# Kernel tuning notes

Measured on AMD Instinct MI355X. Metric: run time of the kernel, lower is better.

Reference implementation:

```python
import jax, jax.numpy as jnp
import numpy as np

# Config matching init_kwargs: N=4 networks, dims 128 -> 1024 -> 1024 -> 512
A, B, D = 8, 2048, 128     # agents, batch, input size
N = 4                       # number of independent SePS networks
H1, H2, H3 = 1024, 1024, 512


def setup_inputs() -> dict:
    key = jax.random.key(0)
    ks = jax.random.split(key, 6)
    inputs = jax.random.normal(ks[0], (A, B, D), dtype=jnp.float32)  # stacked per-agent obs
    seps_indices = jax.random.randint(ks[1], (B, A), 0, N)           # cluster id per (sample, agent)
    scale = lambda k, shape, fan: jax.random.normal(k, shape, dtype=jnp.float32) * (1.0 / np.sqrt(fan))
    W0 = scale(ks[2], (N, D, H1), D);   b0 = jnp.zeros((N, H1), jnp.float32)
    W1 = scale(ks[3], (N, H1, H2), H1); b1 = jnp.zeros((N, H2), jnp.float32)
    W2 = scale(ks[4], (N, H2, H3), H2); b2 = jnp.zeros((N, H3), jnp.float32)
    return {"inputs": inputs, "seps_indices": seps_indices,
            "W0": W0, "b0": b0, "W1": W1, "b1": b1, "W2": W2, "b2": b2}


def reference(inputs, seps_indices, W0, b0, W1, b1, W2, b2):
    # Run every network densely on the full stacked input, as the torch module does.
    # inputs: [A, B, D]; W*: [N, in, out]
    h = jax.nn.relu(jnp.einsum('abd,ndh->nabh', inputs, W0) + b0[:, None, None, :])
    h = jax.nn.relu(jnp.einsum('nabh,nhk->nabk', h, W1) + b1[:, None, None, :])
    out_all = jnp.einsum('nabk,nko->nabo', h, W2) + b2[:, None, None, :]  # [N, A, B, H3]
    # Gather along the network axis per (agent, sample): seps_indices is [B, A]
    idx = seps_indices.T                              # [A, B]
    a = jnp.arange(inputs.shape[0])[:, None]          # [A, 1]
    b = jnp.arange(inputs.shape[1])[None, :]          # [1, B]
    return out_all[idx, a, b, :]                      # [A, B, H3] (stacked per-agent outputs)
```

## Files before the change

kernel.cpp:

```cpp
#include <hip/hip_runtime.h>
#include <hip/hip_bf16.h>

#define AG 8
#define BT 2048
#define RT (AG*BT)
#define NNET 4
#define D0 128
#define H1 1024
#define H2 1024
#define H3 512

typedef __attribute__((ext_vector_type(8))) short short8;
typedef __attribute__((ext_vector_type(4))) float f32x4;

#define VMWAIT(N) asm volatile("s_waitcnt vmcnt(" #N ")" ::: "memory")

__device__ __forceinline__ float bf2f(unsigned short u){
  return __uint_as_float(((unsigned int)u) << 16);
}
__device__ __forceinline__ unsigned short f2bf(float f){
  unsigned int x = __float_as_uint(f);
  x += 0x7fff + ((x >> 16) & 1);
  return (unsigned short)(x >> 16);
}

__device__ __forceinline__ void gload_lds16(const void* g, void* l){
  __builtin_amdgcn_global_load_lds(
      (const __attribute__((address_space(1))) unsigned int*)g,
      (__attribute__((address_space(3))) unsigned int*)l, 16, 0, 0);
}

__device__ __forceinline__ int bucket_off(const int* counts, int n){
  int s = 0;
  #pragma unroll
  for (int i = 0; i < NNET-1; i++) if (i < n) s += counts[i];
  return s;
}

__global__ void k_init(int* counts){
  if (threadIdx.x < NNET) counts[threadIdx.x] = 0;
}

__global__ __launch_bounds__(256) void k_compact(const int* __restrict__ seps,
                          int* __restrict__ counts, int* __restrict__ rowlist){
  __shared__ int lcount[NNET];
  __shared__ int lbase[NNET];
  int t = blockIdx.x * 256 + threadIdx.x;
  if (threadIdx.x < NNET) lcount[threadIdx.x] = 0;
  __syncthreads();
  int a = t >> 11, b = t & (BT-1);
  int n = seps[b*AG + a];
  int lrank = atomicAdd(&lcount[n], 1);
  __syncthreads();
  if (threadIdx.x < NNET)
    lbase[threadIdx.x] = atomicAdd(&counts[threadIdx.x], lcount[threadIdx.x]);
  __syncthreads();
  rowlist[n*RT + lbase[n] + lrank] = t;
}

template<int K, int NOUT>
__global__ __launch_bounds__(256) void k_transpose(const float* __restrict__ W,
                                                   unsigned short* __restrict__ WT){
  __shared__ float tile[32][33];
  int n = blockIdx.z;
  int k0 = blockIdx.x*32, o0 = blockIdx.y*32;
  const float* Wn = W + (size_t)n*K*NOUT;
  unsigned short* WTn = WT + (size_t)n*NOUT*K;
  int tx = threadIdx.x & 31, ty0 = threadIdx.x >> 5;
  #pragma unroll
  for (int r = 0; r < 32; r += 8)
    tile[ty0 + r][tx] = Wn[(size_t)(k0 + ty0 + r)*NOUT + o0 + tx];
  __syncthreads();
  #pragma unroll
  for (int r = 0; r < 32; r += 8)
    WTn[(size_t)(o0 + ty0 + r)*K + k0 + tx] = f2bf(tile[tx][ty0 + r]);
}

__global__ __launch_bounds__(256) void k_gather0(const float* __restrict__ X,
                          const int* __restrict__ counts,
                          const int* __restrict__ rowlist, unsigned short* __restrict__ X0h){
  int n = blockIdx.y;
  int cnt = counts[n];
  int i = blockIdx.x*16 + (threadIdx.x >> 4);
  if (i >= cnt) return;
  int off = bucket_off(counts, n);
  int orig = rowlist[n*RT + i];
  int c = (threadIdx.x & 15) * 8;
  const float* src = X + (size_t)orig*D0 + c;
  float4 v0 = *(const float4*)src, v1 = *(const float4*)(src+4);
  ushort4 u0, u1;
  u0.x=f2bf(v0.x); u0.y=f2bf(v0.y); u0.z=f2bf(v0.z); u0.w=f2bf(v0.w);
  u1.x=f2bf(v1.x); u1.y=f2bf(v1.y); u1.z=f2bf(v1.z); u1.w=f2bf(v1.w);
  unsigned short* dst = X0h + (size_t)(off + i)*D0 + c;
  *(ushort4*)dst = u0; *(ushort4*)(dst+4) = u1;
}

template<int K, int NOUT, int RELU, int SCATTER>
__global__ __launch_bounds__(256) void k_mlp(
    const unsigned short* __restrict__ X,
    const unsigned short* __restrict__ WT,
    const float* __restrict__ Bias,
    const int* __restrict__ counts,
    const int* __restrict__ rowlist,
    unsigned short* __restrict__ Yh,
    float* __restrict__ Yf)
{
  constexpr int T = K / 32;
  const int n = blockIdx.z;
  const int cnt = counts[n];
  const int i0 = blockIdx.x * 128;
  if (i0 >= cnt) return;
  const int off = bucket_off(counts, n);
  const int bn = blockIdx.y * 128;

  __shared__ __align__(16) unsigned short As[3][128*32];
  __shared__ __align__(16) unsigned short Bs[3][128*32];
  __shared__ int rs[128];

  const int t = threadIdx.x, lane = t & 63, wave = t >> 6;
  const int wm = wave >> 1, wn = wave & 1;
  const int lr = lane & 15, g = lane >> 4;

  if (SCATTER && t < 128) rs[t] = rowlist[n*RT + min(i0 + t, cnt-1)];

  const unsigned short* pA[2]; const unsigned short* pB[2];
  unsigned int ldsoff[2];
  const unsigned short* WTn = WT + (size_t)n * NOUT * K;
  #pragma unroll
  for (int j = 0; j < 2; j++){
    int r  = (j*4 + wave)*16 + (lane >> 2);
    int ps = lane & 3;
    int ls = ps ^ ((r >> 1) & 3);
    int rA = min(i0 + r, cnt-1);
    pA[j] = X   + (size_t)(off + rA)*K + ls*8;
    pB[j] = WTn + (size_t)(bn  + r )*K + ls*8;
    ldsoff[j] = (unsigned)(j*4 + wave) * 512;
  }

  int aoff[4], boff[4];
  #pragma unroll
  for (int i = 0; i < 4; i++){
    int ra = wm*64 + i*16 + lr;
    aoff[i] = ra*32 + (g ^ ((ra>>1)&3))*8;
    int rb = wn*64 + i*16 + lr;
    boff[i] = rb*32 + (g ^ ((rb>>1)&3))*8;
  }

  __syncthreads();

  #pragma unroll
  for (int s = 0; s < 3; ++s){
    #pragma unroll
    for (int j = 0; j < 2; j++){
      gload_lds16(pA[j], &As[s][ldsoff[j]]);
      gload_lds16(pB[j], &Bs[s][ldsoff[j]]);
      pA[j] += 32; pB[j] += 32;
    }
  }

  f32x4 acc[4][4] = {};
  int b = 0;
  for (int ks = 0; ks < T; ++ks){
    if (ks < T-2)       VMWAIT(8);
    else if (ks == T-2) VMWAIT(4);
    else                VMWAIT(0);
    __builtin_amdgcn_s_barrier();

    short8 av[4], bv[4];
    #pragma unroll
    for (int i = 0; i < 4; i++) av[i] = *(const short8*)&As[b][aoff[i]];
    #pragma unroll
    for (int i = 0; i < 4; i++) bv[i] = *(const short8*)&Bs[b][boff[i]];
    asm volatile("s_waitcnt lgkmcnt(0)" ::: "memory");
    __builtin_amdgcn_sched_barrier(0);
    __builtin_amdgcn_s_barrier();

    if (ks + 3 < T){
      #pragma unroll
      for (int j = 0; j < 2; j++){
        gload_lds16(pA[j], &As[b][ldsoff[j]]);
        gload_lds16(pB[j], &Bs[b][ldsoff[j]]);
        pA[j] += 32; pB[j] += 32;
      }
    }

    __builtin_amdgcn_s_setprio(1);
    #pragma unroll
    for (int mi = 0; mi < 4; mi++)
      #pragma unroll
      for (int ni = 0; ni < 4; ni++)
        acc[mi][ni] = __builtin_amdgcn_mfma_f32_16x16x32_bf16(bv[ni], av[mi], acc[mi][ni], 0, 0, 0);
    __builtin_amdgcn_s_setprio(0);

    b = (b == 2) ? 0 : b + 1;
  }

  f32x4 bias4[4];
  #pragma unroll
  for (int ni = 0; ni < 4; ni++)
    bias4[ni] = *(const f32x4*)&Bias[n*NOUT + bn + wn*64 + ni*16 + g*4];

  #pragma unroll
  for (int mi = 0; mi < 4; mi++){
    int rloc = wm*64 + mi*16 + lr;
    int grow = i0 + rloc;
    if (grow < cnt){
      #pragma unroll
      for (int ni = 0; ni < 4; ni++){
        float o[4];
        #pragma unroll
        for (int i = 0; i < 4; i++){
          float v = acc[mi][ni][i] + bias4[ni][i];
          if (RELU) v = fmaxf(v, 0.f);
          o[i] = v;
        }
        int cb = bn + wn*64 + ni*16 + (g<<2);
        if (SCATTER){
          *(float4*)&Yf[(size_t)rs[rloc]*NOUT + cb] = make_float4(o[0],o[1],o[2],o[3]);
        } else {
          ushort4 u;
          u.x=f2bf(o[0]); u.y=f2bf(o[1]); u.z=f2bf(o[2]); u.w=f2bf(o[3]);
          *(ushort4*)&Yh[(size_t)(off + grow)*NOUT + cb] = u;
        }
      }
    }
  }
}

extern "C" void kernel_launch(void* const* d_in, const int* in_sizes, int n_in,
                              void* d_out, int out_size, void* d_ws, size_t ws_size,
                              hipStream_t stream) {
  const float* inputs = (const float*)d_in[0];
  const int*   seps   = (const int*)  d_in[1];
  const float* W0     = (const float*)d_in[2];
  const float* b0     = (const float*)d_in[3];
  const float* W1     = (const float*)d_in[4];
  const float* b1     = (const float*)d_in[5];
  const float* W2     = (const float*)d_in[6];
  const float* b2     = (const float*)d_in[7];
  float* out = (float*)d_out;

  char* ws = (char*)d_ws;
  int* counts  = (int*)ws;
  int* rowlist = (int*)(ws + 4096);
  const size_t MB = 1u << 20;
  unsigned short* WT0 = (unsigned short*)(ws + 1*MB);
  unsigned short* WT1 = (unsigned short*)(ws + 2*MB);
  unsigned short* WT2 = (unsigned short*)(ws + 10*MB);
  unsigned short* h1  = (unsigned short*)(ws + 14*MB);
  unsigned short* h2  = (unsigned short*)(ws + 46*MB);
  unsigned short* X0h = (unsigned short*)(ws + 46*MB);

  k_init   <<<1, 64, 0, stream>>>(counts);
  k_compact<<<RT/256, 256, 0, stream>>>(seps, counts, rowlist);

  k_transpose<D0, H1><<<dim3(D0/32, H1/32, NNET), 256, 0, stream>>>(W0, WT0);
  k_transpose<H1, H2><<<dim3(H1/32, H2/32, NNET), 256, 0, stream>>>(W1, WT1);
  k_transpose<H2, H3><<<dim3(H2/32, H3/32, NNET), 256, 0, stream>>>(W2, WT2);
  k_gather0<<<dim3(RT/16, NNET), 256, 0, stream>>>(inputs, counts, rowlist, X0h);

  k_mlp<D0, H1, 1, 0><<<dim3(RT/128, H1/128, NNET), 256, 0, stream>>>(
      X0h, WT0, b0, counts, rowlist, h1, nullptr);
  k_mlp<H1, H2, 1, 0><<<dim3(RT/128, H2/128, NNET), 256, 0, stream>>>(
      h1, WT1, b1, counts, rowlist, h2, nullptr);
  k_mlp<H2, H3, 0, 1><<<dim3(RT/128, H3/128, NNET), 256, 0, stream>>>(
      h2, WT2, b2, counts, rowlist, nullptr, out);
}
```

Measured before the change: 152.1 us.

## Enlarge GEMM tiles to 256-row blocks with 8 waves and templated warp layout

Generalizes the grouped MLP GEMM kernel to 512-thread blocks covering 256 rows and a configurable 256- or 128-column tile, with a templated wave grid and per-thread load counts. Layers 1 and 2 use 256x256 tiles with a 2x4 wave grid, and layer 3 uses 256x128 tiles with 4x2. The aim is more operand reuse from LDS and fewer global loads per MFMA. In exchange it uses more LDS and accumulator registers per block, which can lower occupancy. It also pads more rows in the partial last tile of each network bucket.

```diff
diff --git a/kernel.cpp b/kernel.cpp
--- a/kernel.cpp
+++ b/kernel.cpp
@@ -13,8 +13,6 @@
 typedef __attribute__((ext_vector_type(8))) short short8;
 typedef __attribute__((ext_vector_type(4))) float f32x4;
 
-#define VMWAIT(N) asm volatile("s_waitcnt vmcnt(" #N ")" ::: "memory")
-
 __device__ __forceinline__ float bf2f(unsigned short u){
   return __uint_as_float(((unsigned int)u) << 16);
 }
@@ -22,6 +20,14 @@
   unsigned int x = __float_as_uint(f);
   x += 0x7fff + ((x >> 16) & 1);
   return (unsigned short)(x >> 16);
+}
+
+template<int N> __device__ __forceinline__ void vmw(){
+  if constexpr (N==8)      asm volatile("s_waitcnt vmcnt(8)" ::: "memory");
+  else if constexpr (N==6) asm volatile("s_waitcnt vmcnt(6)" ::: "memory");
+  else if constexpr (N==4) asm volatile("s_waitcnt vmcnt(4)" ::: "memory");
+  else if constexpr (N==3) asm volatile("s_waitcnt vmcnt(3)" ::: "memory");
+  else                     asm volatile("s_waitcnt vmcnt(0)" ::: "memory");
 }
 
 __device__ __forceinline__ void gload_lds16(const void* g, void* l){
@@ -95,8 +101,8 @@
   *(ushort4*)dst = u0; *(ushort4*)(dst+4) = u1;
 }
 
-template<int K, int NOUT, int RELU, int SCATTER>
-__global__ __launch_bounds__(256) void k_mlp(
+template<int K, int NOUT, int BN, int WMW, int WNW, int RELU, int SCATTER>
+__global__ __launch_bounds__(512) void k_mlp(
     const unsigned short* __restrict__ X,
     const unsigned short* __restrict__ WT,
     const float* __restrict__ Bias,
@@ -105,44 +111,57 @@
     unsigned short* __restrict__ Yh,
     float* __restrict__ Yf)
 {
-  constexpr int T = K / 32;
+  constexpr int T  = K / 32;
+  constexpr int MF = 256 / WMW / 16;
+  constexpr int NF = BN  / WNW / 16;
+  constexpr int LA = 2;
+  constexpr int LB = (BN*32*2) / (512*16);
+  constexpr int LPT = LA + LB;
+
   const int n = blockIdx.z;
   const int cnt = counts[n];
-  const int i0 = blockIdx.x * 128;
+  const int i0 = blockIdx.x * 256;
   if (i0 >= cnt) return;
   const int off = bucket_off(counts, n);
-  const int bn = blockIdx.y * 128;
-
-  __shared__ __align__(16) unsigned short As[3][128*32];
-  __shared__ __align__(16) unsigned short Bs[3][128*32];
-  __shared__ int rs[128];
+  const int bn = blockIdx.y * BN;
+
+  __shared__ __align__(16) unsigned short As[3][256*32];
+  __shared__ __align__(16) unsigned short Bs[3][BN*32];
+  __shared__ int rs[256];
 
   const int t = threadIdx.x, lane = t & 63, wave = t >> 6;
-  const int wm = wave >> 1, wn = wave & 1;
+  const int wm = wave / WNW, wn = wave % WNW;
   const int lr = lane & 15, g = lane >> 4;
 
-  if (SCATTER && t < 128) rs[t] = rowlist[n*RT + min(i0 + t, cnt-1)];
-
-  const unsigned short* pA[2]; const unsigned short* pB[2];
-  unsigned int ldsoff[2];
+  if (SCATTER && t < 256) rs[t] = rowlist[n*RT + min(i0 + t, cnt-1)];
+
+  const unsigned short* pA[LA]; const unsigned short* pB[LB];
+  unsigned int loffA[LA], loffB[LB];
   const unsigned short* WTn = WT + (size_t)n * NOUT * K;
   #pragma unroll
-  for (int j = 0; j < 2; j++){
-    int r  = (j*4 + wave)*16 + (lane >> 2);
-    int ps = lane & 3;
-    int ls = ps ^ ((r >> 1) & 3);
-    int rA = min(i0 + r, cnt-1);
-    pA[j] = X   + (size_t)(off + rA)*K + ls*8;
-    pB[j] = WTn + (size_t)(bn  + r )*K + ls*8;
-    ldsoff[j] = (unsigned)(j*4 + wave) * 512;
-  }
-
-  int aoff[4], boff[4];
-  #pragma unroll
-  for (int i = 0; i < 4; i++){
-    int ra = wm*64 + i*16 + lr;
+  for (int j = 0; j < LA; j++){
+    int s = j*512 + t, r = s >> 2;
+    int ls = (s & 3) ^ ((r >> 1) & 3);
+    pA[j] = X + (size_t)(off + min(i0 + r, cnt-1))*K + ls*8;
+    loffA[j] = (unsigned)s * 8;
+  }
+  #pragma unroll
+  for (int j = 0; j < LB; j++){
+    int s = j*512 + t, r = s >> 2;
+    int ls = (s & 3) ^ ((r >> 1) & 3);
+    pB[j] = WTn + (size_t)(bn + r)*K + ls*8;
+    loffB[j] = (unsigned)s * 8;
+  }
+
+  int aoff[MF], boff[NF];
+  #pragma unroll
+  for (int i = 0; i < MF; i++){
+    int ra = wm*(MF*16) + i*16 + lr;
     aoff[i] = ra*32 + (g ^ ((ra>>1)&3))*8;
-    int rb = wn*64 + i*16 + lr;
+  }
+  #pragma unroll
+  for (int i = 0; i < NF; i++){
+    int rb = wn*(NF*16) + i*16 + lr;
     boff[i] = rb*32 + (g ^ ((rb>>1)&3))*8;
   }
 
@@ -151,62 +170,58 @@
   #pragma unroll
   for (int s = 0; s < 3; ++s){
     #pragma unroll
-    for (int j = 0; j < 2; j++){
-      gload_lds16(pA[j], &As[s][ldsoff[j]]);
-      gload_lds16(pB[j], &Bs[s][ldsoff[j]]);
-      pA[j] += 32; pB[j] += 32;
-    }
-  }
-
-  f32x4 acc[4][4] = {};
+    for (int j = 0; j < LA; j++){ gload_lds16(pA[j], &As[s][loffA[j]]); pA[j] += 32; }
+    #pragma unroll
+    for (int j = 0; j < LB; j++){ gload_lds16(pB[j], &Bs[s][loffB[j]]); pB[j] += 32; }
+  }
+
+  f32x4 acc[MF][NF] = {};
   int b = 0;
   for (int ks = 0; ks < T; ++ks){
-    if (ks < T-2)       VMWAIT(8);
-    else if (ks == T-2) VMWAIT(4);
-    else                VMWAIT(0);
+    if (ks < T-2)       vmw<2*LPT>();
+    else if (ks == T-2) vmw<LPT>();
+    else                vmw<0>();
     __builtin_amdgcn_s_barrier();
 
-    short8 av[4], bv[4];
-    #pragma unroll
-    for (int i = 0; i < 4; i++) av[i] = *(const short8*)&As[b][aoff[i]];
-    #pragma unroll
-    for (int i = 0; i < 4; i++) bv[i] = *(const short8*)&Bs[b][boff[i]];
+    short8 av[MF], bv[NF];
+    #pragma unroll
+    for (int i = 0; i < MF; i++) av[i] = *(const short8*)&As[b][aoff[i]];
+    #pragma unroll
+    for (int i = 0; i < NF; i++) bv[i] = *(const short8*)&Bs[b][boff[i]];
     asm volatile("s_waitcnt lgkmcnt(0)" ::: "memory");
     __builtin_amdgcn_sched_barrier(0);
     __builtin_amdgcn_s_barrier();
 
     if (ks + 3 < T){
       #pragma unroll
-      for (int j = 0; j < 2; j++){
-        gload_lds16(pA[j], &As[b][ldsoff[j]]);
-        gload_lds16(pB[j], &Bs[b][ldsoff[j]]);
-        pA[j] += 32; pB[j] += 32;
-      }
+      for (int j = 0; j < LA; j++){ gload_lds16(pA[j], &As[b][loffA[j]]); pA[j] += 32; }
+      #pragma unroll
+      for (int j = 0; j < LB; j++){ gload_lds16(pB[j], &Bs[b][loffB[j]]); pB[j] += 32; }
     }
 
     __builtin_amdgcn_s_setprio(1);
     #pragma unroll
-    for (int mi = 0; mi < 4; mi++)
-      #pragma unroll
-      for (int ni = 0; ni < 4; ni++)
+    for (int mi = 0; mi < MF; mi++)
+      #pragma unroll
+      for (int ni = 0; ni < NF; ni++)
         acc[mi][ni] = __builtin_amdgcn_mfma_f32_16x16x32_bf16(bv[ni], av[mi], acc[mi][ni], 0, 0, 0);
     __builtin_amdgcn_s_setprio(0);
 
     b = (b == 2) ? 0 : b + 1;
   }
 
-  f32x4 bias4[4];
-  #pragma unroll
-  for (int ni = 0; ni < 4; ni++)
-    bias4[ni] = *(const f32x4*)&Bias[n*NOUT + bn + wn*64 + ni*16 + g*4];
-
-  #pragma unroll
-  for (int mi = 0; mi < 4; mi++){
-    int rloc = wm*64 + mi*16 + lr;
+  f32x4 bias4[NF];
+  #pragma unroll
+  for (int ni = 0; ni < NF; ni++)
+    bias4[ni] = *(const f32x4*)&Bias[n*NOUT + bn + wn*(NF*16) + ni*16 + (g<<2)];
+
+  #pragma unroll
+  for (int mi = 0; mi < MF; mi++){
+    int rloc = wm*(MF*16) + mi*16 + lr;
     int grow = i0 + rloc;
     if (grow < cnt){
       #pragma unroll
-      for (int ni = 0; ni < 4; ni++){
+      for (int ni = 0; ni < NF; ni++){
         float o[4];
         #pragma unroll
         for (int i = 0; i < 4; i++){
@@ -214,7 +229,7 @@
           if (RELU) v = fmaxf(v, 0.f);
           o[i] = v;
         }
-        int cb = bn + wn*64 + ni*16 + (g<<2);
+        int cb = bn + wn*(NF*16) + ni*16 + (g<<2);
         if (SCATTER){
           *(float4*)&Yf[(size_t)rs[rloc]*NOUT + cb] = make_float4(o[0],o[1],o[2],o[3]);
         } else {
@@ -259,10 +274,10 @@
   k_transpose<H2, H3><<<dim3(H2/32, H3/32, NNET), 256, 0, stream>>>(W2, WT2);
   k_gather0<<<dim3(RT/16, NNET), 256, 0, stream>>>(inputs, counts, rowlist, X0h);
 
-  k_mlp<D0, H1, 1, 0><<<dim3(RT/128, H1/128, NNET), 256, 0, stream>>>(
+  k_mlp<D0, H1, 256, 2, 4, 1, 0><<<dim3(RT/256, H1/256, NNET), 512, 0, stream>>>(
       X0h, WT0, b0, counts, rowlist, h1, nullptr);
-  k_mlp<H1, H2, 1, 0><<<dim3(RT/128, H2/128, NNET), 256, 0, stream>>>(
+  k_mlp<H1, H2, 256, 2, 4, 1, 0><<<dim3(RT/256, H2/256, NNET), 512, 0, stream>>>(
       h1, WT1, b1, counts, rowlist, h2, nullptr);
-  k_mlp<H2, H3, 0, 1><<<dim3(RT/128, H3/128, NNET), 256, 0, stream>>>(
+  k_mlp<H2, H3, 128, 4, 2, 0, 1><<<dim3(RT/256, H3/128, NNET), 512, 0, stream>>>(
       h2, WT2, b2, counts, rowlist, nullptr, out);
 }
```

Measured after the change: 170.8 us. 1.12x slower.
